# Kernel optimization log

Measured on AMD Instinct MI355X. Metric: run time of the kernel, lower is better.

Reference implementation:

```python
import jax, jax.numpy as jnp
import numpy as np

B, S, D, NQ, NS, QN, SN, KC = 128, 128, 100, 50000, 500, 4, 4, 4
RK, HOPS = 10, 3
NEG = -1e9  # masked attention logit (exp -> 0)


def _lin(x, W, b):
    return x @ W.T + b


def _gru(x, h, W_ih, W_hh, b_ih, b_hh):
    # torch.nn.GRUCell math
    gi = _lin(x, W_ih, b_ih)
    gh = _lin(h, W_hh, b_hh)
    i_r, i_z, i_n = jnp.split(gi, 3, axis=-1)
    h_r, h_z, h_n = jnp.split(gh, 3, axis=-1)
    r = jax.nn.sigmoid(i_r + h_r)
    z = jax.nn.sigmoid(i_z + h_z)
    n = jnp.tanh(i_n + r * h_n)
    return (1.0 - z) * n + z * h


def _forward(Eq, Ec, Er, W_ih1, W_hh1, b_ih1, b_hh1, W_ih2, W_hh2, b_ih2, b_hh2,
             Wagg, bagg, W_last, b_last, W_query, b_query, W_key, b_key, W_W, b_W,
             h1_init, h2_init, question, response, mask, q_neighbors, s_neighbors,
             concept_idx, concept_mask):
    Bb, Ss = question.shape
    Dd = Eq.shape[1]
    # detached keys for the rank-k retrieval (matches .clone().detach())
    K_all = jax.lax.stop_gradient(Eq[question])  # [B,S,D]
    pos = jnp.arange(Ss)
    Wq_part, Wk_part = W_W[0, :Dd], W_W[0, Dd:]

    def aggregate(q_t):
        # multi-hop neighbor gather: q->s->q->s, embed alternately, then
        # triangular mean-aggregation sweep with shared per-hop MLPs
        idx = q_t
        levels = [idx]
        for i in range(HOPS):
            idx = (q_neighbors if i % 2 == 0 else s_neighbors)[idx]
            levels.append(idx)
        embs = [(Eq if i % 2 == 0 else Ec)[ix] for i, ix in enumerate(levels)]
        for i in range(HOPS):
            for j in range(HOPS - i):
                embs[j] = jnp.tanh(_lin(embs[j + 1].mean(-2) + embs[j], Wagg[j], bagg[j]))
        return jnp.tanh(_lin(embs[0], W_last, b_last))

    def predict(qc, states, valid):
        # qc [B,KC+1,D], states [B,RK+1,D], valid [RK+1]
        og = jnp.einsum('bqd,bsd->bqs', qc, states)
        Kt = jnp.tanh(_lin(states, W_query, b_query))
        Qt = jnp.tanh(_lin(qc, W_key, b_key))
        tmp = (jnp.einsum('bqd,d->bq', Qt, Wq_part)[:, :, None]
               + jnp.einsum('bsd,d->bs', Kt, Wk_part)[:, None, :] + b_W[0])
        tmp = jnp.where(valid[None, None, :], tmp, NEG)
        alpha = jax.nn.softmax(tmp, axis=2)
        return jnp.sum(alpha * og, axis=(1, 2))

    def step(carry, xs):
        h1, h2, hist, yhat = carry
        t, q_t, r_t, m_t, q_next = xs
        # masked rows use GNN-aggregated question emb, others the raw emb
        emb_q = jnp.where((m_t != 0)[:, None], aggregate(q_t), Eq[q_t])
        h1n = _gru(jnp.concatenate([emb_q, Er[r_t]], axis=1), h1, W_ih1, W_hh1, b_ih1, b_hh1)
        g2 = _gru(h1n, h2, W_ih2, W_hh2, b_ih2, b_hh2)
        # question + zero-padded related-concept embeddings
        emb_qn = Eq[q_next]
        emb_c = Ec[concept_idx[q_next]] * concept_mask[q_next][..., None]
        qc = jnp.concatenate([emb_qn[:, None, :], emb_c], axis=1)
        # rank-k history retrieval on detached embeddings
        scores = jnp.einsum('bsd,bd->bs', K_all, jax.lax.stop_gradient(emb_qn))
        scores = jnp.where(pos[None, :] < t, scores, -jnp.inf)
        _, top_idx = jax.lax.top_k(scores, RK)
        sel = jnp.take_along_axis(hist, top_idx[..., None], axis=1)
        use_topk = t > RK
        hist_states = jnp.where(use_topk, sel, hist[:, :RK])
        states = jnp.concatenate([g2[:, None, :], hist_states], axis=1)
        valid = jnp.concatenate([jnp.ones((1,), bool),
                                 jnp.where(use_topk, True, pos[:RK] < t)])
        p = predict(qc, states, valid)
        # t==0 writes y_hat[:,0]; t>=1 writes y_hat[:,t+1] (column 1 stays 0)
        col = jnp.where(t == 0, 0, t + 1)
        yhat = yhat + p[:, None] * jax.nn.one_hot(col, Ss, dtype=yhat.dtype)
        # original skips h2/history update at t==0 (continue)
        h2n = jnp.where(t == 0, h2, g2)
        histn = jnp.where(t == 0, hist,
                          jax.lax.dynamic_update_slice(hist, g2[:, None, :], (0, t, 0)))
        return (h1n, h2n, histn, yhat), None

    init = (h1_init, h2_init,
            jnp.zeros((Bb, Ss, Dd), jnp.float32), jnp.zeros((Bb, Ss), jnp.float32))
    xs = (jnp.arange(Ss - 1), question[:, :-1].T, response[:, :-1].T,
          mask[:, :-1].T, question[:, 1:].T)
    (_, _, _, yhat), _ = jax.lax.scan(step, init, xs)
    return yhat


def setup_inputs():
    key = jax.random.key(0)
    ks = jax.random.split(key, 32)
    f = lambda i, shape: (jax.random.normal(ks[i], shape) * 0.05).astype(jnp.float32)
    return {
        'Eq': f(0, (NQ, D)), 'Ec': f(1, (NS, D)), 'Er': f(2, (2, D)),
        'W_ih1': f(3, (3 * D, 2 * D)), 'W_hh1': f(4, (3 * D, D)),
        'b_ih1': f(5, (3 * D,)), 'b_hh1': f(6, (3 * D,)),
        'W_ih2': f(7, (3 * D, D)), 'W_hh2': f(8, (3 * D, D)),
        'b_ih2': f(9, (3 * D,)), 'b_hh2': f(10, (3 * D,)),
        'Wagg': f(11, (HOPS, D, D)), 'bagg': f(12, (HOPS, D)),
        'W_last': f(13, (D, D)), 'b_last': f(14, (D,)),
        'W_query': f(15, (D, D)), 'b_query': f(16, (D,)),
        'W_key': f(17, (D, D)), 'b_key': f(18, (D,)),
        'W_W': f(19, (1, 2 * D)), 'b_W': f(20, (1,)),
        'h1_init': f(21, (B, D)), 'h2_init': f(22, (B, D)),
        'question': jax.random.randint(ks[23], (B, S), 0, NQ),
        'response': jax.random.randint(ks[24], (B, S), 0, 2),
        'mask': jax.random.randint(ks[25], (B, S), 0, 2),
        'q_neighbors': jax.random.randint(ks[26], (NQ, QN), 0, NS),
        's_neighbors': jax.random.randint(ks[27], (NS, SN), 0, NQ),
        'concept_idx': jax.random.randint(ks[28], (NQ, KC), 0, NS),
        'concept_mask': jnp.concatenate(
            [jnp.ones((NQ, 1), bool),
             jax.random.randint(ks[29], (NQ, KC - 1), 0, 2).astype(bool)], axis=1),
    }


def reference(Eq, Ec, Er, W_ih1, W_hh1, b_ih1, b_hh1, W_ih2, W_hh2, b_ih2, b_hh2,
              Wagg, bagg, W_last, b_last, W_query, b_query, W_key, b_key, W_W, b_W,
              h1_init, h2_init, question, response, mask, q_neighbors, s_neighbors,
              concept_idx, concept_mask):
    return _forward(Eq, Ec, Er, W_ih1, W_hh1, b_ih1, b_hh1, W_ih2, W_hh2, b_ih2, b_hh2,
                    Wagg, bagg, W_last, b_last, W_query, b_query, W_key, b_key, W_W, b_W,
                    h1_init, h2_init, question, response, mask, q_neighbors, s_neighbors,
                    concept_idx, concept_mask)
```

## Files before the change

kernel.cpp:

```cpp
#include <hip/hip_runtime.h>
#include <hip/hip_bf16.h>
#include <math.h>

typedef unsigned int u32;

#define B_ 128
#define S_ 128
#define T_ 127
#define D_ 100
#define QN_ 4
#define SN_ 4
#define KC_ 4
#define RK_ 10
#define NEGV -1000000000.0f

__device__ __forceinline__ float sigmf(float x) { return 1.0f / (1.0f + expf(-x)); }

__device__ __forceinline__ u32 f2bfbits(float x) {
  __hip_bfloat16 h = __float2bfloat16(x);
  unsigned short s;
  __builtin_memcpy(&s, &h, 2);
  return (u32)s;
}

__global__ __launch_bounds__(256) void setupk(
    const float* Er, const float* W_ih1, const float* b_ih1,
    const float* Wagg, const float* W_last, const float* W_key,
    const float* b_query, const float* W_W, const float* W_query,
    const float* W_hh1, const float* W_hh2, const float* W_ih2,
    const float* b_hh1, const float* b_hh2, const float* b_ih2,
    float* wih1aT, float* erw, float* waggT, float* wlastT, float* wkeyT,
    float* scal, u32* wcat16, float* bcat)
{
  int gid = blockIdx.x * blockDim.x + threadIdx.x;
  int gsz = gridDim.x * blockDim.x;

  for (int x = gid; x < 30000; x += gsz) {
    int j = x / 300, i = x % 300;
    wih1aT[j * 300 + i] = W_ih1[i * 200 + j];
  }
  for (int x = gid; x < 600; x += gsz) {
    int r = x / 300, i = x % 300;
    float acc = b_ih1[i];
    for (int j = 0; j < 100; j++) acc += Er[r * 100 + j] * W_ih1[i * 200 + 100 + j];
    erw[x] = acc;
  }
  for (int x = gid; x < 30000; x += gsz) {
    int h = x / 10000, rr = x % 10000, j = rr / 100, i = rr % 100;
    waggT[h * 10000 + j * 100 + i] = Wagg[h * 10000 + i * 100 + j];
  }
  for (int x = gid; x < 10000; x += gsz) {
    int j = x / 100, i = x % 100;
    wlastT[j * 100 + i] = W_last[i * 100 + j];
    wkeyT[j * 100 + i] = W_key[i * 100 + j];
  }
  for (int x = gid; x < 114688; x += gsz) {
    int slot = x / 64, rem = x % 64, sbu = rem / 16, k = rem % 16;
    const float* src = nullptr;
    if (slot < 300)                       src = W_hh1 + (size_t)slot * 100;
    else if (slot < 600)                  src = W_hh2 + (size_t)(slot - 300) * 100;
    else if (slot >= 1024 && slot < 1324) src = W_ih2 + (size_t)(slot - 1024) * 100;
    else if (slot >= 1536 && slot < 1636) src = W_query + (size_t)(slot - 1536) * 100;
    u32 lo = 0, hi = 0;
    if (src) {
      int e0 = 2 * k, e1 = 2 * k + 1;
      if (e0 < 25) lo = f2bfbits(src[sbu * 25 + e0]);
      if (e1 < 25) hi = f2bfbits(src[sbu * 25 + e1]);
    }
    wcat16[x] = (hi << 16) | lo;
  }
  for (int x = gid; x < 1792; x += gsz) {
    float v = 0.f;
    if (x < 300) v = b_hh1[x];
    else if (x < 600) v = b_hh2[x - 300];
    else if (x >= 1024 && x < 1324) v = b_ih2[x - 1024];
    else if (x >= 1536 && x < 1636) v = b_query[x - 1536];
    bcat[x] = v;
  }
  if (gid == 0) {
    float acc = 0.f;
    for (int i = 0; i < 100; i++) acc += tanhf(b_query[i]) * W_W[100 + i];
    scal[0] = acc;
  }
}

__global__ __launch_bounds__(256) void phaseA(
    const float* Eq, const float* Ec, const int* question, const int* response, const int* mask,
    const int* qnb, const int* snb,
    const float* wih1aT, const float* erw, const float* waggT, const float* wlastT,
    const float* baggf, const float* blastf, float* gi1_all)
{
  const int t = blockIdx.x, b = blockIdx.y, tid = threadIdx.x;
  __shared__ float e0[100], ne0[100], e1[400], ne1[400];
  __shared__ float e2[1600], ne2[1600], m3[1600];
  __shared__ float sum4[400], sum1[100], emq[100];
  __shared__ int l1[4], l2[16], l3[64];

  const int qt = question[b * S_ + t];
  const int mt = mask[b * S_ + t];
  const int rt = response[b * S_ + t];

  if (mt != 0) {
    if (tid < 4) l1[tid] = qnb[qt * QN_ + tid];
    for (int x = tid; x < 100; x += 256) e0[x] = Eq[(size_t)qt * 100 + x];
    __syncthreads();
    if (tid < 16) l2[tid] = snb[l1[tid >> 2] * SN_ + (tid & 3)];
    for (int x = tid; x < 400; x += 256) e1[x] = Ec[(size_t)l1[x / 100] * 100 + (x % 100)];
    __syncthreads();
    if (tid < 64) l3[tid] = qnb[l2[tid >> 2] * QN_ + (tid & 3)];
    for (int x = tid; x < 1600; x += 256) e2[x] = Eq[(size_t)l2[x / 100] * 100 + (x % 100)];
    __syncthreads();
    for (int x = tid; x < 1600; x += 256) {
      int r = x / 100, j = x % 100;
      const int* lr = l3 + r * 4;
      float s = Ec[(size_t)lr[0] * 100 + j] + Ec[(size_t)lr[1] * 100 + j] +
                Ec[(size_t)lr[2] * 100 + j] + Ec[(size_t)lr[3] * 100 + j];
      m3[x] = e2[x] + 0.25f * s;
    }
    for (int x = tid; x < 100; x += 256)
      sum1[x] = e0[x] + 0.25f * (e1[x] + e1[100 + x] + e1[200 + x] + e1[300 + x]);
    for (int x = tid; x < 400; x += 256) {
      int k = x / 100, j = x % 100;
      const float* e2k = e2 + k * 400;
      sum4[x] = e1[x] + 0.25f * (e2k[j] + e2k[100 + j] + e2k[200 + j] + e2k[300 + j]);
    }
    __syncthreads();
    for (int o = tid; o < 2100; o += 256) {
      const float *in, *W;
      float bia;
      float* dst;
      int i = o % 100;
      if (o < 100)      { in = sum1;                           W = waggT;          bia = baggf[i];       dst = ne0 + o; }
      else if (o < 500) { in = sum4 + ((o - 100) / 100) * 100; W = waggT + 10000;  bia = baggf[100 + i]; dst = ne1 + (o - 100); }
      else              { in = m3 + ((o - 500) / 100) * 100;   W = waggT + 20000;  bia = baggf[200 + i]; dst = ne2 + (o - 500); }
      float acc = bia;
      for (int j = 0; j < 100; j++) acc += in[j] * W[j * 100 + i];
      *dst = tanhf(acc);
    }
    __syncthreads();
    for (int x = tid; x < 100; x += 256)
      sum1[x] = ne0[x] + 0.25f * (ne1[x] + ne1[100 + x] + ne1[200 + x] + ne1[300 + x]);
    for (int x = tid; x < 400; x += 256) {
      int k = x / 100, j = x % 100;
      const float* n2k = ne2 + k * 400;
      sum4[x] = ne1[x] + 0.25f * (n2k[j] + n2k[100 + j] + n2k[200 + j] + n2k[300 + j]);
    }
    __syncthreads();
    for (int o = tid; o < 500; o += 256) {
      int i = o % 100;
      if (o < 100) {
        float acc = baggf[i];
        for (int j = 0; j < 100; j++) acc += sum1[j] * waggT[j * 100 + i];
        e0[i] = tanhf(acc);
      } else {
        const float* in = sum4 + ((o - 100) / 100) * 100;
        float acc = baggf[100 + i];
        for (int j = 0; j < 100; j++) acc += in[j] * waggT[10000 + j * 100 + i];
        e1[o - 100] = tanhf(acc);
      }
    }
    __syncthreads();
    for (int x = tid; x < 100; x += 256)
      sum1[x] = e0[x] + 0.25f * (e1[x] + e1[100 + x] + e1[200 + x] + e1[300 + x]);
    __syncthreads();
    for (int o = tid; o < 100; o += 256) {
      float acc = baggf[o];
      for (int j = 0; j < 100; j++) acc += sum1[j] * waggT[j * 100 + o];
      ne0[o] = tanhf(acc);
    }
    __syncthreads();
    for (int o = tid; o < 100; o += 256) {
      float acc = blastf[o];
      for (int j = 0; j < 100; j++) acc += ne0[j] * wlastT[j * 100 + o];
      emq[o] = tanhf(acc);
    }
    __syncthreads();
  } else {
    for (int x = tid; x < 100; x += 256) emq[x] = Eq[(size_t)qt * 100 + x];
    __syncthreads();
  }

  const size_t bt = (size_t)b * T_ + t;
  for (int o = tid; o < 300; o += 256) {
    float acc = erw[rt * 300 + o];
    for (int j = 0; j < 100; j++) acc += emq[j] * wih1aT[j * 300 + o];
    gi1_all[bt * 300 + o] = acc;
  }
}

__global__ __launch_bounds__(128) void phaseB(
    const float* Eq, const float* Ec, const int* question, const int* cidx, const int* cmask,
    const float* wkeyT, const float* b_key, const float* W_W,
    float* qw_all, int* top10_all)
{
  const int t = blockIdx.x, b = blockIdx.y, tid = threadIdx.x;
  const size_t bt = (size_t)b * T_ + t;
  __shared__ float qcf[500];
  __shared__ float qtl[500];
  __shared__ float qwp[20];
  __shared__ float orig[128];
  __shared__ float sval[128];
  __shared__ int sidx[128];
  __shared__ int ci[4], cm[4];

  const int qn = question[b * S_ + t + 1];
  if (tid < 4) { ci[tid] = cidx[qn * KC_ + tid]; cm[tid] = cmask[qn * KC_ + tid]; }
  __syncthreads();

  for (int u = tid; u < 500; u += 128) {
    int row = u / 100, j = u % 100;
    float v;
    if (row == 0) v = Eq[(size_t)qn * 100 + j];
    else {
      int k = row - 1;
      v = cm[k] ? Ec[(size_t)ci[k] * 100 + j] : 0.f;
    }
    qcf[u] = v;
  }
  __syncthreads();
  for (int o = tid; o < 500; o += 128) {
    int q = o / 100, i = o % 100;
    float acc = b_key[i];
    const float* src = qcf + q * 100;
    for (int j = 0; j < 100; j++) acc += src[j] * wkeyT[j * 100 + i];
    qtl[o] = tanhf(acc);
  }
  __syncthreads();
  if (tid < 20) {
    int q = tid / 4, part = tid % 4;
    float acc = 0.f;
    for (int j = part * 25; j < part * 25 + 25; j++) acc += qtl[q * 100 + j] * W_W[j];
    qwp[tid] = acc;
  }
  __syncthreads();
  if (tid < 5) qw_all[bt * 5 + tid] = qwp[tid * 4] + qwp[tid * 4 + 1] + qwp[tid * 4 + 2] + qwp[tid * 4 + 3];

  if (t > RK_) {
    float sc = -__builtin_inff();
    if (tid < t) {
      int qs = question[b * S_ + tid];
      float acc = 0.f;
      for (int j = 0; j < 100; j++) acc += Eq[(size_t)qs * 100 + j] * qcf[j];
      sc = acc;
    }
    orig[tid] = sc;
    __syncthreads();
    for (int pass = 0; pass < 10; pass++) {
      sval[tid] = orig[tid];
      sidx[tid] = tid;
      __syncthreads();
      for (int offt = 64; offt > 0; offt >>= 1) {
        if (tid < offt) {
          float v2 = sval[tid + offt];
          int i2 = sidx[tid + offt];
          if (v2 > sval[tid] || (v2 == sval[tid] && i2 < sidx[tid])) { sval[tid] = v2; sidx[tid] = i2; }
        }
        __syncthreads();
      }
      if (tid == 0) top10_all[bt * 10 + pass] = sidx[0];
      if (tid == sidx[0]) orig[tid] = -__builtin_inff();
      __syncthreads();
    }
  }
}

__device__ __forceinline__ float bf16_dot32(const uint4 w[4], const float hr[32]) {
  float a = 0.f;
#pragma unroll
  for (int c = 0; c < 4; ++c) {
    uint4 ww = w[c];
    const int e = c * 8;
    a = fmaf(__uint_as_float(ww.x << 16),         hr[e + 0], a);
    a = fmaf(__uint_as_float(ww.x & 0xffff0000u), hr[e + 1], a);
    a = fmaf(__uint_as_float(ww.y << 16),         hr[e + 2], a);
    a = fmaf(__uint_as_float(ww.y & 0xffff0000u), hr[e + 3], a);
    a = fmaf(__uint_as_float(ww.z << 16),         hr[e + 4], a);
    a = fmaf(__uint_as_float(ww.z & 0xffff0000u), hr[e + 5], a);
    a = fmaf(__uint_as_float(ww.w << 16),         hr[e + 6], a);
    a = fmaf(__uint_as_float(ww.w & 0xffff0000u), hr[e + 7], a);
  }
  return a;
}

__global__ __launch_bounds__(1024) void seqk(
    const u32* __restrict__ wcat16, const float* __restrict__ bcat,
    const float* __restrict__ gi1_all, const float* __restrict__ qw_all, const int* __restrict__ top10_all,
    const float* __restrict__ W_W, const float* __restrict__ b_W,
    const float* __restrict__ Eq, const float* __restrict__ Ec, const int* __restrict__ question,
    const int* __restrict__ cidx, const int* __restrict__ cmask,
    const float* __restrict__ h1_init, const float* __restrict__ h2_init, const float* __restrict__ scal,
    float* __restrict__ g2hist_g, float* __restrict__ out)
{
  const int b = blockIdx.x, tid = threadIdx.x;
  const int grp = tid >> 2, sub = tid & 3;
  const int ptid = tid - 424;
  const uint4* wimg = (const uint4*)wcat16;
  float* const g2h = g2hist_g + (size_t)b * (T_ * 128);

  __shared__ float hcomb[200];
  __shared__ __align__(16) float h1n[100], g2v[100];
  __shared__ float gh2[300], kqs[100];
  __shared__ float gi1d[2][300];
  __shared__ float qcd[2][500];
  __shared__ float qwd[2][5];
  __shared__ int topd[2][10];
  __shared__ float kwhist[128];
  __shared__ float ogs[2][55];
  __shared__ float bresS[1000];
  __shared__ float wkS[100];
  __shared__ int cidS[8], cid0S[8];
  __shared__ int qn1S, qnS;
  __shared__ u32 whh1S[300 * 52];
  __shared__ u32 wih2S[300 * 52];
  __shared__ u32 wqS[100 * 52];

  for (int x = tid; x < 1000; x += 1024) {
    int src = (x < 600) ? x : ((x < 900) ? (1024 + (x - 600)) : (1536 + (x - 900)));
    bresS[x] = bcat[src];
  }
  if (tid < 100) wkS[tid] = W_W[100 + tid];

  for (int x = tid; x < 300 * 52; x += 1024) {
    int s = x / 52, r = x - s * 52;
    int sb = r / 13, k = r - sb * 13;
    whh1S[x] = wcat16[(size_t)s * 64 + sb * 16 + k];
    wih2S[x] = wcat16[(size_t)(1024 + s) * 64 + sb * 16 + k];
  }
  for (int x = tid; x < 100 * 52; x += 1024) {
    int s = x / 52, r = x - s * 52;
    int sb = r / 13, k = r - sb * 13;
    wqS[x] = wcat16[(size_t)(1536 + s) * 64 + sb * 16 + k];
  }

  const float bWv = b_W[0];
  const float kw0 = scal[0];

  if (tid < 100) {
    hcomb[tid] = h1_init[b * 100 + tid];
  } else if (tid < 200) {
    hcomb[tid] = h2_init[b * 100 + (tid - 100)];
  }
  if (tid >= 200 && tid < 328) g2h[tid - 200] = 0.f;
  if (tid < 128) kwhist[tid] = kw0;
  if (tid < 300) gi1d[0][tid] = gi1_all[(size_t)b * T_ * 300 + tid];
  if (tid >= 300 && tid < 305) qwd[0][tid - 300] = qw_all[(size_t)b * T_ * 5 + (tid - 300)];
  if (tid == 306) { qn1S = question[b * S_ + 2]; qnS = question[b * S_ + 3]; }
  if (tid >= 320 && tid < 328) {
    int k = tid - 320, qn0 = question[b * S_ + 1];
    cid0S[k] = (k < 4) ? cidx[qn0 * KC_ + k] : cmask[qn0 * KC_ + k - 4];
  }
  if (tid >= 328 && tid < 336) {
    int k = tid - 328, qn1 = question[b * S_ + 2];
    cidS[k] = (k < 4) ? cidx[qn1 * KC_ + k] : cmask[qn1 * KC_ + k - 4];
  }
  __syncthreads();
  if (tid < 500) {
    int q = tid / 100, j = tid % 100;
    int qn0 = question[b * S_ + 1];
    qcd[0][tid] = (q == 0) ? Eq[(size_t)qn0 * 100 + j]
                           : (cid0S[4 + q - 1] ? Ec[(size_t)cid0S[q - 1] * 100 + j] : 0.f);
  }
  __syncthreads();

  for (int t = 0; t < T_; ++t) {
    const size_t bt = (size_t)b * T_ + t;
    const int cur = t & 1, nxt = cur ^ 1;
    const bool pf = (t + 1) < T_;
    const int qn1 = qn1S, qn2 = qnS;

    float pqc = 0.f, pgi = 0.f, pqw = 0.f;
    int ptop = 0, pci = 0, pqn = 0;
    if (pf) {
      if (ptid >= 0 && ptid < 500) {
        int q = ptid / 100, j = ptid % 100;
        pqc = (q == 0) ? Eq[(size_t)qn1 * 100 + j]
                       : (cidS[4 + q - 1] ? Ec[(size_t)cidS[q - 1] * 100 + j] : 0.f);
      }
      if (ptid >= 0 && ptid < 300) pgi = gi1_all[(bt + 1) * 300 + ptid];
      if (tid >= 924 && tid < 929) pqw = qw_all[(bt + 1) * 5 + (tid - 924)];
      if (tid >= 929 && tid < 939 && (t + 1) > RK_) ptop = top10_all[(bt + 1) * 10 + (tid - 929)];
      if (tid >= 939 && tid < 947 && (t + 2) < T_) {
        int k = tid - 939;
        pci = (k < 4) ? cidx[qn2 * KC_ + k] : cmask[qn2 * KC_ + k - 4];
      }
      if (tid == 947) pqn = question[b * S_ + min(t + 4, S_ - 1)];
    }

    if (grp < 100) {
      const int j = grp;
      const u32* wr0 = whh1S + j * 52 + sub * 13;
      const u32* wr1 = wr0 + 100 * 52;
      const u32* wr2 = wr0 + 200 * 52;
      const float* hsrc = hcomb + sub * 25;
      float a0 = 0.f, a1 = 0.f, a2 = 0.f;
#pragma unroll
      for (int k = 0; k < 13; ++k) {
        float h0  = hsrc[2 * k];
        float h1v = (2 * k + 1 < 25) ? hsrc[2 * k + 1] : 0.f;
        u32 w0v = wr0[k], w1v = wr1[k], w2v = wr2[k];
        a0 = fmaf(__uint_as_float(w0v << 16),         h0,  a0);
        a0 = fmaf(__uint_as_float(w0v & 0xffff0000u), h1v, a0);
        a1 = fmaf(__uint_as_float(w1v << 16),         h0,  a1);
        a1 = fmaf(__uint_as_float(w1v & 0xffff0000u), h1v, a1);
        a2 = fmaf(__uint_as_float(w2v << 16),         h0,  a2);
        a2 = fmaf(__uint_as_float(w2v & 0xffff0000u), h1v, a2);
      }
      a0 += __shfl_xor(a0, 1); a0 += __shfl_xor(a0, 2);
      a1 += __shfl_xor(a1, 1); a1 += __shfl_xor(a1, 2);
      a2 += __shfl_xor(a2, 1); a2 += __shfl_xor(a2, 2);
      if (sub == 0) {
        float g0 = a0 + bresS[j], gg1 = a1 + bresS[100 + j], gg2 = a2 + bresS[200 + j];
        float rg = sigmf(gi1d[cur][j] + g0);
        float z  = sigmf(gi1d[cur][100 + j] + gg1);
        float n  = tanhf(gi1d[cur][200 + j] + rg * gg2);
        h1n[j] = (1.f - z) * n + z * hcomb[j];
      }
    } else if (grp >= 128 && grp < 228) {
      const int j = grp - 128;
      const int s0 = 300 + j;
      uint4 w0[4], w1[4], w2[4];
      {
        const uint4* p0 = wimg + (size_t)s0 * 16 + sub * 4;
        const uint4* p1 = wimg + (size_t)(s0 + 100) * 16 + sub * 4;
        const uint4* p2 = wimg + (size_t)(s0 + 200) * 16 + sub * 4;
#pragma unroll
        for (int c = 0; c < 4; ++c) { w0[c] = p0[c]; w1[c] = p1[c]; w2[c] = p2[c]; }
      }
      float hr[32];
#pragma unroll
      for (int c = 25; c < 32; ++c) hr[c] = 0.f;
#pragma unroll
      for (int c = 0; c < 25; ++c) hr[c] = hcomb[100 + sub * 25 + c];
      float a0 = bf16_dot32(w0, hr);
      float a1 = bf16_dot32(w1, hr);
      float a2 = bf16_dot32(w2, hr);
      a0 += __shfl_xor(a0, 1); a0 += __shfl_xor(a0, 2);
      a1 += __shfl_xor(a1, 1); a1 += __shfl_xor(a1, 2);
      a2 += __shfl_xor(a2, 1); a2 += __shfl_xor(a2, 2);
      if (sub == 0) {
        gh2[j]       = a0 + bresS[300 + j];
        gh2[100 + j] = a1 + bresS[400 + j];
        gh2[200 + j] = a2 + bresS[500 + j];
      }
    }
    __syncthreads();

    if (grp < 100) {
      const int j = grp;
      const u32* wr0 = wih2S + j * 52 + sub * 13;
      const u32* wr1 = wr0 + 100 * 52;
      const u32* wr2 = wr0 + 200 * 52;
      const float* hsrc = h1n + sub * 25;
      float a0 = 0.f, a1 = 0.f, a2 = 0.f;
#pragma unroll
      for (int k = 0; k < 13; ++k) {
        float h0  = hsrc[2 * k];
        float h1v = (2 * k + 1 < 25) ? hsrc[2 * k + 1] : 0.f;
        u32 w0v = wr0[k], w1v = wr1[k], w2v = wr2[k];
        a0 = fmaf(__uint_as_float(w0v << 16),         h0,  a0);
        a0 = fmaf(__uint_as_float(w0v & 0xffff0000u), h1v, a0);
        a1 = fmaf(__uint_as_float(w1v << 16),         h0,  a1);
        a1 = fmaf(__uint_as_float(w1v & 0xffff0000u), h1v, a1);
        a2 = fmaf(__uint_as_float(w2v << 16),         h0,  a2);
        a2 = fmaf(__uint_as_float(w2v & 0xffff0000u), h1v, a2);
      }
      a0 += __shfl_xor(a0, 1); a0 += __shfl_xor(a0, 2);
      a1 += __shfl_xor(a1, 1); a1 += __shfl_xor(a1, 2);
      a2 += __shfl_xor(a2, 1); a2 += __shfl_xor(a2, 2);
      if (sub == 0) {
        float i_r = a0 + bresS[600 + j], i_z = a1 + bresS[700 + j], i_n = a2 + bresS[800 + j];
        float rg = sigmf(i_r + gh2[j]);
        float z  = sigmf(i_z + gh2[100 + j]);
        float n  = tanhf(i_n + rg * gh2[200 + j]);
        g2v[j] = (1.f - z) * n + z * hcomb[100 + j];
      }
    } else if (tid >= 400 && tid < 500) {
      hcomb[tid - 400] = h1n[tid - 400];
    } else if (grp >= 128 && grp < 178) {
      int d = grp - 128;
      int s = 1 + d / 5, q = d % 5;
      bool valid = (t > RK_) || (s - 1 < t);
      float a = 0.f;
      if (valid) {
        int idx = (t > RK_) ? topd[cur][s - 1] : (s - 1);
        const float* qcr = &qcd[cur][q * 100 + sub * 25];
        const float* hrow = g2h + (size_t)idx * 128 + sub * 25;
#pragma unroll
        for (int c = 0; c < 25; ++c) a = fmaf(qcr[c], hrow[c], a);
      }
      a += __shfl_xor(a, 1);
      a += __shfl_xor(a, 2);
      if (sub == 0) ogs[cur][s * 5 + q] = a;
    }
    __syncthreads();

    if (grp < 100) {
      const u32* wq = wqS + grp * 52 + sub * 13;
      const float* hsrc = g2v + sub * 25;
      float a = 0.f;
#pragma unroll
      for (int k = 0; k < 13; ++k) {
        float h0  = hsrc[2 * k];
        float h1v = (2 * k + 1 < 25) ? hsrc[2 * k + 1] : 0.f;
        u32 wv = wq[k];
        a = fmaf(__uint_as_float(wv << 16),         h0,  a);
        a = fmaf(__uint_as_float(wv & 0xffff0000u), h1v, a);
      }
      a += __shfl_xor(a, 1);
      a += __shfl_xor(a, 2);
      if (sub == 0) kqs[grp] = tanhf(a + bresS[900 + grp]) * wkS[grp];
    } else if (grp < 105) {
      int q = grp - 100;
      const float* qcr = &qcd[cur][q * 100 + sub * 25];
      float a = 0.f;
#pragma unroll
      for (int c = 0; c < 25; ++c) a = fmaf(qcr[c], g2v[sub * 25 + c], a);
      a += __shfl_xor(a, 1);
      a += __shfl_xor(a, 2);
      if (sub == 0) ogs[cur][q] = a;
    }
    if (ptid >= 0) {
      if (pf) {
        if (ptid < 500) qcd[nxt][ptid] = pqc;
        if (ptid < 300) gi1d[nxt][ptid] = pgi;
        if (tid >= 924 && tid < 929) qwd[nxt][tid - 924] = pqw;
        if (tid >= 929 && tid < 939 && (t + 1) > RK_) topd[nxt][tid - 929] = min(T_ - 1, max(0, ptop));
        if (tid >= 939 && tid < 947 && (t + 2) < T_) cidS[tid - 939] = pci;
        if (tid == 947) { qn1S = qn2; qnS = pqn; }
      }
      if (t > 0 && ptid < 100) {
        hcomb[100 + ptid] = g2v[ptid];
        g2h[(size_t)t * 128 + ptid] = g2v[ptid];
      }
    }
    __syncthreads();

    if (tid < 64) {
      float v = (tid < 50) ? (kqs[tid] + kqs[tid + 50]) : 0.f;
      v += __shfl_xor(v, 1);
      v += __shfl_xor(v, 2);
      v += __shfl_xor(v, 4);
      v += __shfl_xor(v, 8);
      v += __shfl_xor(v, 16);
      v += __shfl_xor(v, 32);
      const float kw = v;
      float pq = 0.f;
      if (tid < 5) {
        const float qw = qwd[cur][tid];
        float tmp[11];
        float m = -__builtin_inff();
#pragma unroll
        for (int s = 0; s < 11; ++s) {
          float kws;
          bool valid;
          if (s == 0) { kws = kw; valid = true; }
          else if (t > RK_) { kws = kwhist[topd[cur][s - 1]]; valid = true; }
          else { valid = (s - 1 < t); kws = kwhist[s - 1]; }
          float tv = valid ? (qw + kws + bWv) : NEGV;
          tmp[s] = tv;
          m = fmaxf(m, tv);
        }
        float den = 0.f, num = 0.f;
#pragma unroll
        for (int s = 0; s < 11; ++s) {
          float e = expf(tmp[s] - m);
          den += e;
          num += e * ogs[cur][s * 5 + tid];
        }
        pq = num / den;
      }
      if (tid == 5 && t > 0) kwhist[t] = kw;
      float sp = pq;
      sp += __shfl_xor(sp, 1);
      sp += __shfl_xor(sp, 2);
      sp += __shfl_xor(sp, 4);
      if (tid == 0) {
        int col = (t == 0) ? 0 : (t + 1);
        out[b * S_ + col] = sp;
        if (t == 0) out[b * S_ + 1] = 0.f;
      }
    }
  }
}

extern "C" void kernel_launch(void* const* d_in, const int* in_sizes, int n_in,
                              void* d_out, int out_size, void* d_ws, size_t ws_size,
                              hipStream_t stream)
{
  (void)in_sizes; (void)n_in; (void)out_size; (void)ws_size;
  const float* Eq     = (const float*)d_in[0];
  const float* Ec     = (const float*)d_in[1];
  const float* Er     = (const float*)d_in[2];
  const float* W_ih1  = (const float*)d_in[3];
  const float* W_hh1  = (const float*)d_in[4];
  const float* b_ih1  = (const float*)d_in[5];
  const float* b_hh1  = (const float*)d_in[6];
  const float* W_ih2  = (const float*)d_in[7];
  const float* W_hh2  = (const float*)d_in[8];
  const float* b_ih2  = (const float*)d_in[9];
  const float* b_hh2  = (const float*)d_in[10];
  const float* Wagg   = (const float*)d_in[11];
  const float* bagg   = (const float*)d_in[12];
  const float* W_last = (const float*)d_in[13];
  const float* b_last = (const float*)d_in[14];
  const float* W_query= (const float*)d_in[15];
  const float* b_query= (const float*)d_in[16];
  const float* W_key  = (const float*)d_in[17];
  const float* b_key  = (const float*)d_in[18];
  const float* W_W    = (const float*)d_in[19];
  const float* b_W    = (const float*)d_in[20];
  const float* h1_init= (const float*)d_in[21];
  const float* h2_init= (const float*)d_in[22];
  const int* question = (const int*)d_in[23];
  const int* response = (const int*)d_in[24];
  const int* mask     = (const int*)d_in[25];
  const int* qnb      = (const int*)d_in[26];
  const int* snb      = (const int*)d_in[27];
  const int* cidx     = (const int*)d_in[28];
  const int* cmask    = (const int*)d_in[29];
  float* out = (float*)d_out;

  char* ws = (char*)d_ws;
  size_t off = 0;
  auto alloc = [&](size_t bytes) -> void* {
    void* p = ws + off;
    off += (bytes + 255) & ~(size_t)255;
    return p;
  };
  float* wih1aT = (float*)alloc(30000 * 4);
  float* erw    = (float*)alloc(600 * 4);
  float* waggT  = (float*)alloc(30000 * 4);
  float* wlastT = (float*)alloc(10000 * 4);
  float* wkeyT  = (float*)alloc(10000 * 4);
  float* scal   = (float*)alloc(4);
  u32*   wcat16 = (u32*)alloc(114688 * 4);
  float* bcat   = (float*)alloc(1792 * 4);
  float* gi1_all = (float*)alloc((size_t)B_ * T_ * 300 * 4);
  float* qw_all  = (float*)alloc((size_t)B_ * T_ * 5 * 4);
  int*   top10   = (int*)alloc((size_t)B_ * T_ * 10 * 4);
  float* g2h     = (float*)alloc((size_t)B_ * T_ * 128 * 4);

  hipLaunchKernelGGL(setupk, dim3(128), dim3(256), 0, stream,
      Er, W_ih1, b_ih1, Wagg, W_last, W_key, b_query, W_W, W_query,
      W_hh1, W_hh2, W_ih2, b_hh1, b_hh2, b_ih2,
      wih1aT, erw, waggT, wlastT, wkeyT, scal, wcat16, bcat);

  hipLaunchKernelGGL(phaseA, dim3(T_, B_), dim3(256), 0, stream,
      Eq, Ec, question, response, mask, qnb, snb,
      wih1aT, erw, waggT, wlastT, bagg, b_last, gi1_all);

  hipLaunchKernelGGL(phaseB, dim3(T_, B_), dim3(128), 0, stream,
      Eq, Ec, question, cidx, cmask, wkeyT, b_key, W_W,
      qw_all, top10);

  hipLaunchKernelGGL(seqk, dim3(B_), dim3(1024), 0, stream,
      wcat16, bcat, gi1_all, qw_all, top10, W_W, b_W,
      Eq, Ec, question, cidx, cmask,
      h1_init, h2_init, scal, g2h, out);
}
```

Before: 1.397 ms.

## Software-pipeline GRU layers across timesteps to drop one barrier per step

Restructures the per-step recurrence so the layer-1 GRU for step t+1 and the layer-2 hidden projection for step t+1 are computed one phase ahead, alongside the layer-2 input GRU of step t. This removes one __syncthreads phase per timestep by double-buffering h1 and prefetching gi1 two steps ahead. The og dot products move to otherwise idle thread ranges with two lanes per output. The cost is more complex indexing and a prologue step, with some risk of a stale-buffer hazard.

New measurement: 1.411 ms. About the same (+1.0%).

```diff
diff --git a/kernel.cpp b/kernel.cpp
--- a/kernel.cpp
+++ b/kernel.cpp
@@ -297,8 +297,9 @@
   const uint4* wimg = (const uint4*)wcat16;
   float* const g2h = g2hist_g + (size_t)b * (T_ * 128);
 
-  __shared__ float hcomb[200];
-  __shared__ __align__(16) float h1n[100], g2v[100];
+  __shared__ float h1d[2][100];
+  __shared__ float h2S[100];
+  __shared__ __align__(16) float g2v[100];
   __shared__ float gh2[300], kqs[100];
   __shared__ float gi1d[2][300];
   __shared__ float qcd[2][500];
@@ -334,38 +335,99 @@
 
   const float bWv = b_W[0];
   const float kw0 = scal[0];
+  const size_t bbase = (size_t)b * T_ * 300;
 
   if (tid < 100) {
-    hcomb[tid] = h1_init[b * 100 + tid];
+    h1d[1][tid] = h1_init[b * 100 + tid];
   } else if (tid < 200) {
-    hcomb[tid] = h2_init[b * 100 + (tid - 100)];
+    h2S[tid - 100] = h2_init[b * 100 + (tid - 100)];
   }
   if (tid >= 200 && tid < 328) g2h[tid - 200] = 0.f;
   if (tid < 128) kwhist[tid] = kw0;
-  if (tid < 300) gi1d[0][tid] = gi1_all[(size_t)b * T_ * 300 + tid];
-  if (tid >= 300 && tid < 305) qwd[0][tid - 300] = qw_all[(size_t)b * T_ * 5 + (tid - 300)];
-  if (tid == 306) { qn1S = question[b * S_ + 2]; qnS = question[b * S_ + 3]; }
-  if (tid >= 320 && tid < 328) {
-    int k = tid - 320, qn0 = question[b * S_ + 1];
+  if (tid < 300) gi1d[1][tid] = gi1_all[bbase + tid];
+  if (tid >= 300 && tid < 600) gi1d[0][tid - 300] = gi1_all[bbase + 300 + (tid - 300)];
+  if (tid >= 600 && tid < 605) qwd[0][tid - 600] = qw_all[(size_t)b * T_ * 5 + (tid - 600)];
+  if (tid == 606) { qn1S = question[b * S_ + 2]; qnS = question[b * S_ + 3]; }
+  if (tid >= 620 && tid < 628) {
+    int k = tid - 620, qn0 = question[b * S_ + 1];
     cid0S[k] = (k < 4) ? cidx[qn0 * KC_ + k] : cmask[qn0 * KC_ + k - 4];
   }
-  if (tid >= 328 && tid < 336) {
-    int k = tid - 328, qn1 = question[b * S_ + 2];
+  if (tid >= 628 && tid < 636) {
+    int k = tid - 628, qn1 = question[b * S_ + 2];
     cidS[k] = (k < 4) ? cidx[qn1 * KC_ + k] : cmask[qn1 * KC_ + k - 4];
   }
   __syncthreads();
+
   if (tid < 500) {
     int q = tid / 100, j = tid % 100;
     int qn0 = question[b * S_ + 1];
     qcd[0][tid] = (q == 0) ? Eq[(size_t)qn0 * 100 + j]
                            : (cid0S[4 + q - 1] ? Ec[(size_t)cid0S[q - 1] * 100 + j] : 0.f);
   }
+  if (grp < 100) {
+    const int j = grp;
+    const u32* wr0 = whh1S + j * 52 + sub * 13;
+    const u32* wr1 = wr0 + 100 * 52;
+    const u32* wr2 = wr0 + 200 * 52;
+    const float* hsrc = h1d[1] + sub * 25;
+    float a0 = 0.f, a1 = 0.f, a2 = 0.f;
+#pragma unroll
+    for (int k = 0; k < 13; ++k) {
+      float h0  = hsrc[2 * k];
+      float h1v = (2 * k + 1 < 25) ? hsrc[2 * k + 1] : 0.f;
+      u32 w0v = wr0[k], w1v = wr1[k], w2v = wr2[k];
+      a0 = fmaf(__uint_as_float(w0v << 16),         h0,  a0);
+      a0 = fmaf(__uint_as_float(w0v & 0xffff0000u), h1v, a0);
+      a1 = fmaf(__uint_as_float(w1v << 16),         h0,  a1);
+      a1 = fmaf(__uint_as_float(w1v & 0xffff0000u), h1v, a1);
+      a2 = fmaf(__uint_as_float(w2v << 16),         h0,  a2);
+      a2 = fmaf(__uint_as_float(w2v & 0xffff0000u), h1v, a2);
+    }
+    a0 += __shfl_xor(a0, 1); a0 += __shfl_xor(a0, 2);
+    a1 += __shfl_xor(a1, 1); a1 += __shfl_xor(a1, 2);
+    a2 += __shfl_xor(a2, 1); a2 += __shfl_xor(a2, 2);
+    if (sub == 0) {
+      float g0 = a0 + bresS[j], gg1 = a1 + bresS[100 + j], gg2 = a2 + bresS[200 + j];
+      float rg = sigmf(gi1d[1][j] + g0);
+      float z  = sigmf(gi1d[1][100 + j] + gg1);
+      float n  = tanhf(gi1d[1][200 + j] + rg * gg2);
+      h1d[0][j] = (1.f - z) * n + z * h1d[1][j];
+    }
+  } else if (grp >= 128 && grp < 228) {
+    const int j = grp - 128;
+    const int s0 = 300 + j;
+    uint4 w0[4], w1[4], w2[4];
+    {
+      const uint4* p0 = wimg + (size_t)s0 * 16 + sub * 4;
+      const uint4* p1 = wimg + (size_t)(s0 + 100) * 16 + sub * 4;
+      const uint4* p2 = wimg + (size_t)(s0 + 200) * 16 + sub * 4;
+#pragma unroll
+      for (int c = 0; c < 4; ++c) { w0[c] = p0[c]; w1[c] = p1[c]; w2[c] = p2[c]; }
+    }
+    float hr[32];
+#pragma unroll
+    for (int c = 25; c < 32; ++c) hr[c] = 0.f;
+#pragma unroll
+    for (int c = 0; c < 25; ++c) hr[c] = h2S[sub * 25 + c];
+    float a0 = bf16_dot32(w0, hr);
+    float a1 = bf16_dot32(w1, hr);
+    float a2 = bf16_dot32(w2, hr);
+    a0 += __shfl_xor(a0, 1); a0 += __shfl_xor(a0, 2);
+    a1 += __shfl_xor(a1, 1); a1 += __shfl_xor(a1, 2);
+    a2 += __shfl_xor(a2, 1); a2 += __shfl_xor(a2, 2);
+    if (sub == 0) {
+      gh2[j]       = a0 + bresS[300 + j];
+      gh2[100 + j] = a1 + bresS[400 + j];
+      gh2[200 + j] = a2 + bresS[500 + j];
+    }
+  }
   __syncthreads();
 
   for (int t = 0; t < T_; ++t) {
     const size_t bt = (size_t)b * T_ + t;
     const int cur = t & 1, nxt = cur ^ 1;
     const bool pf = (t + 1) < T_;
+    const bool pf2 = (t + 2) < T_;
     const int qn1 = qn1S, qn2 = qnS;
 
     float pqc = 0.f, pgi = 0.f, pqw = 0.f;
@@ -376,22 +438,24 @@
         pqc = (q == 0) ? Eq[(size_t)qn1 * 100 + j]
                        : (cidS[4 + q - 1] ? Ec[(size_t)cidS[q - 1] * 100 + j] : 0.f);
       }
-      if (ptid >= 0 && ptid < 300) pgi = gi1_all[(bt + 1) * 300 + ptid];
       if (tid >= 924 && tid < 929) pqw = qw_all[(bt + 1) * 5 + (tid - 924)];
       if (tid >= 929 && tid < 939 && (t + 1) > RK_) ptop = top10_all[(bt + 1) * 10 + (tid - 929)];
-      if (tid >= 939 && tid < 947 && (t + 2) < T_) {
+      if (tid == 947) pqn = question[b * S_ + min(t + 4, S_ - 1)];
+    }
+    if (pf2) {
+      if (ptid >= 0 && ptid < 300) pgi = gi1_all[(bt + 2) * 300 + ptid];
+      if (tid >= 939 && tid < 947) {
         int k = tid - 939;
         pci = (k < 4) ? cidx[qn2 * KC_ + k] : cmask[qn2 * KC_ + k - 4];
       }
-      if (tid == 947) pqn = question[b * S_ + min(t + 4, S_ - 1)];
     }
 
     if (grp < 100) {
       const int j = grp;
-      const u32* wr0 = whh1S + j * 52 + sub * 13;
+      const u32* wr0 = wih2S + j * 52 + sub * 13;
       const u32* wr1 = wr0 + 100 * 52;
       const u32* wr2 = wr0 + 200 * 52;
-      const float* hsrc = hcomb + sub * 25;
+      const float* hsrc = h1d[cur] + sub * 25;
       float a0 = 0.f, a1 = 0.f, a2 = 0.f;
 #pragma unroll
       for (int k = 0; k < 13; ++k) {
@@ -409,93 +473,49 @@
       a1 += __shfl_xor(a1, 1); a1 += __shfl_xor(a1, 2);
       a2 += __shfl_xor(a2, 1); a2 += __shfl_xor(a2, 2);
       if (sub == 0) {
-        float g0 = a0 + bresS[j], gg1 = a1 + bresS[100 + j], gg2 = a2 + bresS[200 + j];
-        float rg = sigmf(gi1d[cur][j] + g0);
-        float z  = sigmf(gi1d[cur][100 + j] + gg1);
-        float n  = tanhf(gi1d[cur][200 + j] + rg * gg2);
-        h1n[j] = (1.f - z) * n + z * hcomb[j];
-      }
-    } else if (grp >= 128 && grp < 228) {
-      const int j = grp - 128;
-      const int s0 = 300 + j;
-      uint4 w0[4], w1[4], w2[4];
-      {
-        const uint4* p0 = wimg + (size_t)s0 * 16 + sub * 4;
-        const uint4* p1 = wimg + (size_t)(s0 + 100) * 16 + sub * 4;
-        const uint4* p2 = wimg + (size_t)(s0 + 200) * 16 + sub * 4;
-#pragma unroll
-        for (int c = 0; c < 4; ++c) { w0[c] = p0[c]; w1[c] = p1[c]; w2[c] = p2[c]; }
-      }
-      float hr[32];
-#pragma unroll
-      for (int c = 25; c < 32; ++c) hr[c] = 0.f;
-#pragma unroll
-      for (int c = 0; c < 25; ++c) hr[c] = hcomb[100 + sub * 25 + c];
-      float a0 = bf16_dot32(w0, hr);
-      float a1 = bf16_dot32(w1, hr);
-      float a2 = bf16_dot32(w2, hr);
-      a0 += __shfl_xor(a0, 1); a0 += __shfl_xor(a0, 2);
-      a1 += __shfl_xor(a1, 1); a1 += __shfl_xor(a1, 2);
-      a2 += __shfl_xor(a2, 1); a2 += __shfl_xor(a2, 2);
-      if (sub == 0) {
-        gh2[j]       = a0 + bresS[300 + j];
-        gh2[100 + j] = a1 + bresS[400 + j];
-        gh2[200 + j] = a2 + bresS[500 + j];
-      }
-    }
-    __syncthreads();
-
-    if (grp < 100) {
-      const int j = grp;
-      const u32* wr0 = wih2S + j * 52 + sub * 13;
-      const u32* wr1 = wr0 + 100 * 52;
-      const u32* wr2 = wr0 + 200 * 52;
-      const float* hsrc = h1n + sub * 25;
-      float a0 = 0.f, a1 = 0.f, a2 = 0.f;
-#pragma unroll
-      for (int k = 0; k < 13; ++k) {
-        float h0  = hsrc[2 * k];
-        float h1v = (2 * k + 1 < 25) ? hsrc[2 * k + 1] : 0.f;
-        u32 w0v = wr0[k], w1v = wr1[k], w2v = wr2[k];
-        a0 = fmaf(__uint_as_float(w0v << 16),         h0,  a0);
-        a0 = fmaf(__uint_as_float(w0v & 0xffff0000u), h1v, a0);
-        a1 = fmaf(__uint_as_float(w1v << 16),         h0,  a1);
-        a1 = fmaf(__uint_as_float(w1v & 0xffff0000u), h1v, a1);
-        a2 = fmaf(__uint_as_float(w2v << 16),         h0,  a2);
-        a2 = fmaf(__uint_as_float(w2v & 0xffff0000u), h1v, a2);
-      }
-      a0 += __shfl_xor(a0, 1); a0 += __shfl_xor(a0, 2);
-      a1 += __shfl_xor(a1, 1); a1 += __shfl_xor(a1, 2);
-      a2 += __shfl_xor(a2, 1); a2 += __shfl_xor(a2, 2);
-      if (sub == 0) {
         float i_r = a0 + bresS[600 + j], i_z = a1 + bresS[700 + j], i_n = a2 + bresS[800 + j];
         float rg = sigmf(i_r + gh2[j]);
         float z  = sigmf(i_z + gh2[100 + j]);
         float n  = tanhf(i_n + rg * gh2[200 + j]);
-        g2v[j] = (1.f - z) * n + z * hcomb[100 + j];
-      }
-    } else if (tid >= 400 && tid < 500) {
-      hcomb[tid - 400] = h1n[tid - 400];
-    } else if (grp >= 128 && grp < 178) {
-      int d = grp - 128;
-      int s = 1 + d / 5, q = d % 5;
-      bool valid = (t > RK_) || (s - 1 < t);
-      float a = 0.f;
-      if (valid) {
-        int idx = (t > RK_) ? topd[cur][s - 1] : (s - 1);
-        const float* qcr = &qcd[cur][q * 100 + sub * 25];
-        const float* hrow = g2h + (size_t)idx * 128 + sub * 25;
-#pragma unroll
-        for (int c = 0; c < 25; ++c) a = fmaf(qcr[c], hrow[c], a);
-      }
-      a += __shfl_xor(a, 1);
-      a += __shfl_xor(a, 2);
-      if (sub == 0) ogs[cur][s * 5 + q] = a;
+        g2v[j] = (1.f - z) * n + z * h2S[j];
+      }
+    } else if (grp >= 112 && grp < 212) {
+      if (pf) {
+        const int j = grp - 112;
+        const u32* wr0 = whh1S + j * 52 + sub * 13;
+        const u32* wr1 = wr0 + 100 * 52;
+        const u32* wr2 = wr0 + 200 * 52;
+        const float* hsrc = h1d[cur] + sub * 25;
+        float a0 = 0.f, a1 = 0.f, a2 = 0.f;
+#pragma unroll
+        for (int k = 0; k < 13; ++k) {
+          float h0  = hsrc[2 * k];
+          float h1v = (2 * k + 1 < 25) ? hsrc[2 * k + 1] : 0.f;
+          u32 w0v = wr0[k], w1v = wr1[k], w2v = wr2[k];
+          a0 = fmaf(__uint_as_float(w0v << 16),         h0,  a0);
+          a0 = fmaf(__uint_as_float(w0v & 0xffff0000u), h1v, a0);
+          a1 = fmaf(__uint_as_float(w1v << 16),         h0,  a1);
+          a1 = fmaf(__uint_as_float(w1v & 0xffff0000u), h1v, a1);
+          a2 = fmaf(__uint_as_float(w2v << 16),         h0,  a2);
+          a2 = fmaf(__uint_as_float(w2v & 0xffff0000u), h1v, a2);
+        }
+        a0 += __shfl_xor(a0, 1); a0 += __shfl_xor(a0, 2);
+        a1 += __shfl_xor(a1, 1); a1 += __shfl_xor(a1, 2);
+        a2 += __shfl_xor(a2, 1); a2 += __shfl_xor(a2, 2);
+        if (sub == 0) {
+          float g0 = a0 + bresS[j], gg1 = a1 + bresS[100 + j], gg2 = a2 + bresS[200 + j];
+          float rg = sigmf(gi1d[cur][j] + g0);
+          float z  = sigmf(gi1d[cur][100 + j] + gg1);
+          float n  = tanhf(gi1d[cur][200 + j] + rg * gg2);
+          h1d[nxt][j] = (1.f - z) * n + z * h1d[cur][j];
+        }
+      }
     }
     __syncthreads();
 
     if (grp < 100) {
-      const u32* wq = wqS + grp * 52 + sub * 13;
+      const int j = grp;
+      const u32* wq = wqS + j * 52 + sub * 13;
       const float* hsrc = g2v + sub * 25;
       float a = 0.f;
 #pragma unroll
@@ -508,7 +528,7 @@
       }
       a += __shfl_xor(a, 1);
       a += __shfl_xor(a, 2);
-      if (sub == 0) kqs[grp] = tanhf(a + bresS[900 + grp]) * wkS[grp];
+      if (sub == 0) kqs[j] = tanhf(a + bresS[900 + j]) * wkS[j];
     } else if (grp < 105) {
       int q = grp - 100;
       const float* qcr = &qcd[cur][q * 100 + sub * 25];
@@ -518,18 +538,74 @@
       a += __shfl_xor(a, 1);
       a += __shfl_xor(a, 2);
       if (sub == 0) ogs[cur][q] = a;
+    } else if (grp >= 128 && grp < 228) {
+      if (pf) {
+        const int j = grp - 128;
+        const int s0 = 300 + j;
+        uint4 w0[4], w1[4], w2[4];
+        {
+          const uint4* p0 = wimg + (size_t)s0 * 16 + sub * 4;
+          const uint4* p1 = wimg + (size_t)(s0 + 100) * 16 + sub * 4;
+          const uint4* p2 = wimg + (size_t)(s0 + 200) * 16 + sub * 4;
+#pragma unroll
+          for (int c = 0; c < 4; ++c) { w0[c] = p0[c]; w1[c] = p1[c]; w2[c] = p2[c]; }
+        }
+        float hr[32];
+#pragma unroll
+        for (int c = 25; c < 32; ++c) hr[c] = 0.f;
+        const float* h2src = (t == 0) ? (h2S + sub * 25) : (g2v + sub * 25);
+#pragma unroll
+        for (int c = 0; c < 25; ++c) hr[c] = h2src[c];
+        float a0 = bf16_dot32(w0, hr);
+        float a1 = bf16_dot32(w1, hr);
+        float a2 = bf16_dot32(w2, hr);
+        a0 += __shfl_xor(a0, 1); a0 += __shfl_xor(a0, 2);
+        a1 += __shfl_xor(a1, 1); a1 += __shfl_xor(a1, 2);
+        a2 += __shfl_xor(a2, 1); a2 += __shfl_xor(a2, 2);
+        if (sub == 0) {
+          gh2[j]       = a0 + bresS[300 + j];
+          gh2[100 + j] = a1 + bresS[400 + j];
+          gh2[200 + j] = a2 + bresS[500 + j];
+        }
+      }
+    }
+    {
+      int ogl = -1;
+      if (tid >= 448 && tid < 512) ogl = tid - 448;
+      else if (tid >= 960 && tid < 996) ogl = 64 + (tid - 960);
+      if (ogl >= 0 && ogl < 100) {
+        int d = ogl >> 1, sub2 = ogl & 1;
+        int s = 1 + d / 5, q = d % 5;
+        bool valid = (t > RK_) || (s - 1 < t);
+        float a = 0.f;
+        if (valid) {
+          int idx = (t > RK_) ? topd[cur][s - 1] : (s - 1);
+          const float* qcr = &qcd[cur][q * 100 + sub2 * 50];
+          const float* hrow = g2h + (size_t)idx * 128 + sub2 * 50;
+          float aL = 0.f, aH = 0.f;
+#pragma unroll
+          for (int c = 0; c < 25; ++c) aL = fmaf(qcr[c], hrow[c], aL);
+#pragma unroll
+          for (int c = 0; c < 25; ++c) aH = fmaf(qcr[25 + c], hrow[25 + c], aH);
+          a = aL + aH;
+        }
+        a += __shfl_xor(a, 1);
+        if (sub2 == 0) ogs[cur][s * 5 + q] = a;
+      }
     }
     if (ptid >= 0) {
       if (pf) {
         if (ptid < 500) qcd[nxt][ptid] = pqc;
-        if (ptid < 300) gi1d[nxt][ptid] = pgi;
         if (tid >= 924 && tid < 929) qwd[nxt][tid - 924] = pqw;
         if (tid >= 929 && tid < 939 && (t + 1) > RK_) topd[nxt][tid - 929] = min(T_ - 1, max(0, ptop));
-        if (tid >= 939 && tid < 947 && (t + 2) < T_) cidS[tid - 939] = pci;
         if (tid == 947) { qn1S = qn2; qnS = pqn; }
       }
+      if (pf2) {
+        if (ptid < 300) gi1d[nxt][ptid] = pgi;
+        if (tid >= 939 && tid < 947) cidS[tid - 939] = pci;
+      }
       if (t > 0 && ptid < 100) {
-        hcomb[100 + ptid] = g2v[ptid];
+        h2S[ptid] = g2v[ptid];
         g2h[(size_t)t * 128 + ptid] = g2v[ptid];
       }
     }
```

## Vectorize matvecs to two outputs per thread and use wavefront shuffles for top-k

Applied to the files above, without the earlier changes.

The matrix-vector loops in the aggregation phase, the GRU input projection and the key projection now compute two adjacent outputs per thread. They use float2 weight loads and a partially unrolled FMA loop, which halves the loads of the input vector and widens the global weight reads. The top-10 selection in phaseB drops the shared-memory tree reduction, which needed about seven barriers per pass. It now does an in-register butterfly reduction with __shfl_xor across each 64-lane wavefront and combines the two wave results through shared memory. Each pass uses fewer threads for the matvecs, so parallelism drops somewhat, and the result depends on the shuffle reduction keeping the same tie-break as before.

Result: slower. 1.749 ms (+25.1%).

```diff
diff --git a/kernel.cpp b/kernel.cpp
--- a/kernel.cpp
+++ b/kernel.cpp
@@ -125,17 +125,23 @@
       sum4[x] = e1[x] + 0.25f * (e2k[j] + e2k[100 + j] + e2k[200 + j] + e2k[300 + j]);
     }
     __syncthreads();
-    for (int o = tid; o < 2100; o += 256) {
-      const float *in, *W;
-      float bia;
+    for (int it = tid; it < 1050; it += 256) {
+      int row = it / 50, i = (it % 50) * 2;
+      const float *in, *W, *biap;
       float* dst;
-      int i = o % 100;
-      if (o < 100)      { in = sum1;                           W = waggT;          bia = baggf[i];       dst = ne0 + o; }
-      else if (o < 500) { in = sum4 + ((o - 100) / 100) * 100; W = waggT + 10000;  bia = baggf[100 + i]; dst = ne1 + (o - 100); }
-      else              { in = m3 + ((o - 500) / 100) * 100;   W = waggT + 20000;  bia = baggf[200 + i]; dst = ne2 + (o - 500); }
-      float acc = bia;
-      for (int j = 0; j < 100; j++) acc += in[j] * W[j * 100 + i];
-      *dst = tanhf(acc);
+      if (row == 0)      { in = sum1;                    W = waggT;         biap = baggf + i;       dst = ne0 + i; }
+      else if (row < 5)  { in = sum4 + (row - 1) * 100;  W = waggT + 10000; biap = baggf + 100 + i; dst = ne1 + (row - 1) * 100 + i; }
+      else               { in = m3 + (row - 5) * 100;    W = waggT + 20000; biap = baggf + 200 + i; dst = ne2 + (row - 5) * 100 + i; }
+      float a0 = biap[0], a1 = biap[1];
+#pragma unroll 4
+      for (int j = 0; j < 100; ++j) {
+        float iv = in[j];
+        float2 w = *(const float2*)(W + j * 100 + i);
+        a0 = fmaf(iv, w.x, a0);
+        a1 = fmaf(iv, w.y, a1);
+      }
+      dst[0] = tanhf(a0);
+      dst[1] = tanhf(a1);
     }
     __syncthreads();
     for (int x = tid; x < 100; x += 256)
@@ -146,18 +152,22 @@
       sum4[x] = ne1[x] + 0.25f * (n2k[j] + n2k[100 + j] + n2k[200 + j] + n2k[300 + j]);
     }
     __syncthreads();
-    for (int o = tid; o < 500; o += 256) {
-      int i = o % 100;
-      if (o < 100) {
-        float acc = baggf[i];
-        for (int j = 0; j < 100; j++) acc += sum1[j] * waggT[j * 100 + i];
-        e0[i] = tanhf(acc);
-      } else {
-        const float* in = sum4 + ((o - 100) / 100) * 100;
-        float acc = baggf[100 + i];
-        for (int j = 0; j < 100; j++) acc += in[j] * waggT[10000 + j * 100 + i];
-        e1[o - 100] = tanhf(acc);
-      }
+    for (int it = tid; it < 250; it += 256) {
+      int row = it / 50, i = (it % 50) * 2;
+      const float *in, *W, *biap;
+      float* dst;
+      if (row == 0) { in = sum1;                   W = waggT;         biap = baggf + i;       dst = e0 + i; }
+      else          { in = sum4 + (row - 1) * 100; W = waggT + 10000; biap = baggf + 100 + i; dst = e1 + (row - 1) * 100 + i; }
+      float a0 = biap[0], a1 = biap[1];
+#pragma unroll 4
+      for (int j = 0; j < 100; ++j) {
+        float iv = in[j];
+        float2 w = *(const float2*)(W + j * 100 + i);
+        a0 = fmaf(iv, w.x, a0);
+        a1 = fmaf(iv, w.y, a1);
+      }
+      dst[0] = tanhf(a0);
+      dst[1] = tanhf(a1);
     }
     __syncthreads();
     for (int x = tid; x < 100; x += 256)
@@ -181,10 +191,19 @@
   }
 
   const size_t bt = (size_t)b * T_ + t;
-  for (int o = tid; o < 300; o += 256) {
-    float acc = erw[rt * 300 + o];
-    for (int j = 0; j < 100; j++) acc += emq[j] * wih1aT[j * 300 + o];
-    gi1_all[bt * 300 + o] = acc;
+  for (int it = tid; it < 150; it += 256) {
+    int o = it * 2;
+    float2 er = *(const float2*)(erw + rt * 300 + o);
+    float a0 = er.x, a1 = er.y;
+#pragma unroll 4
+    for (int j = 0; j < 100; ++j) {
+      float iv = emq[j];
+      float2 w = *(const float2*)(wih1aT + j * 300 + o);
+      a0 = fmaf(iv, w.x, a0);
+      a1 = fmaf(iv, w.y, a1);
+    }
+    gi1_all[bt * 300 + o] = a0;
+    gi1_all[bt * 300 + o + 1] = a1;
   }
 }
 
@@ -198,9 +217,8 @@
   __shared__ float qcf[500];
   __shared__ float qtl[500];
   __shared__ float qwp[20];
-  __shared__ float orig[128];
-  __shared__ float sval[128];
-  __shared__ int sidx[128];
+  __shared__ float sval[2];
+  __shared__ int sidx[2];
   __shared__ int ci[4], cm[4];
 
   const int qn = question[b * S_ + t + 1];
@@ -218,12 +236,19 @@
     qcf[u] = v;
   }
   __syncthreads();
-  for (int o = tid; o < 500; o += 128) {
-    int q = o / 100, i = o % 100;
-    float acc = b_key[i];
+  for (int it = tid; it < 250; it += 128) {
+    int q = it / 50, i = (it % 50) * 2;
+    float a0 = b_key[i], a1 = b_key[i + 1];
     const float* src = qcf + q * 100;
-    for (int j = 0; j < 100; j++) acc += src[j] * wkeyT[j * 100 + i];
-    qtl[o] = tanhf(acc);
+#pragma unroll 4
+    for (int j = 0; j < 100; ++j) {
+      float iv = src[j];
+      float2 w = *(const float2*)(wkeyT + j * 100 + i);
+      a0 = fmaf(iv, w.x, a0);
+      a1 = fmaf(iv, w.y, a1);
+    }
+    qtl[q * 100 + i] = tanhf(a0);
+    qtl[q * 100 + i + 1] = tanhf(a1);
   }
   __syncthreads();
   if (tid < 20) {
@@ -243,22 +268,22 @@
       for (int j = 0; j < 100; j++) acc += Eq[(size_t)qs * 100 + j] * qcf[j];
       sc = acc;
     }
-    orig[tid] = sc;
-    __syncthreads();
     for (int pass = 0; pass < 10; pass++) {
-      sval[tid] = orig[tid];
-      sidx[tid] = tid;
+      float v = sc;
+      int vi = tid;
+#pragma unroll
+      for (int off = 1; off < 64; off <<= 1) {
+        float v2 = __shfl_xor(v, off);
+        int i2 = __shfl_xor(vi, off);
+        if (v2 > v || (v2 == v && i2 < vi)) { v = v2; vi = i2; }
+      }
+      if ((tid & 63) == 0) { sval[tid >> 6] = v; sidx[tid >> 6] = vi; }
       __syncthreads();
-      for (int offt = 64; offt > 0; offt >>= 1) {
-        if (tid < offt) {
-          float v2 = sval[tid + offt];
-          int i2 = sidx[tid + offt];
-          if (v2 > sval[tid] || (v2 == sval[tid] && i2 < sidx[tid])) { sval[tid] = v2; sidx[tid] = i2; }
-        }
-        __syncthreads();
-      }
-      if (tid == 0) top10_all[bt * 10 + pass] = sidx[0];
-      if (tid == sidx[0]) orig[tid] = -__builtin_inff();
+      float v0 = sval[0], v1 = sval[1];
+      int i0 = sidx[0], i1 = sidx[1];
+      int widx = (v1 > v0 || (v1 == v0 && i1 < i0)) ? i1 : i0;
+      if (tid == 0) top10_all[bt * 10 + pass] = widx;
+      if (tid == widx) sc = -__builtin_inff();
       __syncthreads();
     }
   }
```
